# Performance work log

Measured on AMD Instinct MI355X. Metric: run time of the kernel, lower is better.

The kernel has to match this reference:

```python
import jax, jax.numpy as jnp
import numpy as np

N = 8192
F_IN = 128
F_OUT = 128
BLOCK = 64  # row block for the masked neighbor max-pool (keeps peak mem ~256MB)


def setup_inputs() -> dict:
    key = jax.random.key(0)
    k_in, k_adj, k_w, k_b = jax.random.split(key, 4)
    x = jax.random.normal(k_in, (N, F_IN), dtype=jnp.float32)
    adj = (jax.random.uniform(k_adj, (N, N)) < 0.01).astype(jnp.float32)
    adj = adj.at[jnp.arange(N), jnp.arange(N)].set(1.0)
    stdv = 1.0 / np.sqrt(F_OUT)
    weight = jax.random.uniform(k_w, (F_IN, F_OUT), minval=-stdv, maxval=stdv, dtype=jnp.float32)
    bias = jax.random.uniform(k_b, (F_OUT,), minval=-stdv, maxval=stdv, dtype=jnp.float32)
    return {"input": x, "adj": adj, "weight": weight, "bias": bias}


def _graph_pool(out, adj):
    # For each row i: max over features of out[j] where adj[i, j] != 0.
    # Blocked scan over rows to avoid materializing [N, N, F].
    neg = jnp.asarray(jnp.finfo(out.dtype).min, out.dtype)

    def body(_, adj_blk):  # adj_blk: [BLOCK, N]
        masked = jnp.where(adj_blk[:, :, None] != 0, out[None, :, :], neg)  # [BLOCK, N, F]
        return None, jnp.max(masked, axis=1)

    _, blocks = jax.lax.scan(body, None, adj.reshape(N // BLOCK, BLOCK, N))
    return blocks.reshape(N, out.shape[-1])


def reference(input, adj, weight, bias):
    h = input @ weight                       # [N, F_out]
    out = jnp.maximum(adj @ h + bias, 0.0)   # aggregate + bias + relu
    return _graph_pool(out, adj)             # per-node neighbor max-pool
```

## Files before the change

### kernel.cpp

```cpp
#include <hip/hip_runtime.h>
#include <float.h>

constexpr int N = 8192;
constexpr int F = 128;
constexpr int CAP = 256;

__global__ __launch_bounds__(128) void gemm_xw(const float* __restrict__ x,
                                               const float* __restrict__ w,
                                               float* __restrict__ h) {
    __shared__ float xs[8][F];
    const int f = threadIdx.x;
    const int row0 = blockIdx.x * 8;

    #pragma unroll
    for (int r = 0; r < 8; ++r) xs[r][f] = x[(size_t)(row0 + r) * F + f];
    __syncthreads();

    float acc[8];
    #pragma unroll
    for (int r = 0; r < 8; ++r) acc[r] = 0.f;

    for (int k = 0; k < F; ++k) {
        const float wk = w[(size_t)k * F + f];
        #pragma unroll
        for (int r = 0; r < 8; ++r) acc[r] += xs[r][k] * wk;
    }

    #pragma unroll
    for (int r = 0; r < 8; ++r) h[(size_t)(row0 + r) * F + f] = acc[r];
}

__global__ __launch_bounds__(256) void aggregate_relu_build_csr(
        const float* __restrict__ adj,
        const float* __restrict__ h,
        const float* __restrict__ bias,
        float* __restrict__ out2,
        unsigned short* __restrict__ csr_idx,
        int* __restrict__ csr_cnt) {
    __shared__ int idx[CAP];
    __shared__ int cnt;
    __shared__ float partial[F];

    const int tid  = threadIdx.x;
    const int lane = tid & 63;
    const int row  = blockIdx.x;

    if (tid == 0) cnt = 0;
    __syncthreads();

    const float4* arow = (const float4*)(adj + (size_t)row * N);
    float4 v[8];
    #pragma unroll
    for (int it = 0; it < 8; ++it) v[it] = arow[tid + it * 256];

    const unsigned long long lt = (1ull << lane) - 1ull;
    #pragma unroll
    for (int it = 0; it < 8; ++it) {
        const int j4 = 4 * (tid + it * 256);
        const float4 vv = v[it];
        const unsigned long long m0 = __ballot(vv.x != 0.f);
        const unsigned long long m1 = __ballot(vv.y != 0.f);
        const unsigned long long m2 = __ballot(vv.z != 0.f);
        const unsigned long long m3 = __ballot(vv.w != 0.f);
        const int c0 = __popcll(m0), c1 = __popcll(m1),
                  c2 = __popcll(m2), c3 = __popcll(m3);
        const int tot = c0 + c1 + c2 + c3;
        int base = 0;
        if (lane == 0 && tot) base = atomicAdd(&cnt, tot);
        base = __shfl(base, 0, 64);
        if (vv.x != 0.f) idx[base + __popcll(m0 & lt)] = j4 + 0;
        base += c0;
        if (vv.y != 0.f) idx[base + __popcll(m1 & lt)] = j4 + 1;
        base += c1;
        if (vv.z != 0.f) idx[base + __popcll(m2 & lt)] = j4 + 2;
        base += c2;
        if (vv.w != 0.f) idx[base + __popcll(m3 & lt)] = j4 + 3;
    }
    __syncthreads();

    const int n = min(cnt, CAP);

    if (tid == 0) csr_cnt[row] = n;
    if (tid < n) csr_idx[(size_t)row * CAP + tid] = (unsigned short)idx[tid];

    const int f = tid & (F - 1);
    const int half = tid >> 7;

    float acc = 0.f;
    int e = half;
    for (; e + 6 < n; e += 8) {
        const int j0 = idx[e], j1 = idx[e + 2], j2 = idx[e + 4], j3 = idx[e + 6];
        const float a0 = h[(size_t)j0 * F + f];
        const float a1 = h[(size_t)j1 * F + f];
        const float a2 = h[(size_t)j2 * F + f];
        const float a3 = h[(size_t)j3 * F + f];
        acc += (a0 + a1) + (a2 + a3);
    }
    for (; e < n; e += 2) acc += h[(size_t)idx[e] * F + f];

    if (half == 1) partial[f] = acc;
    __syncthreads();
    if (half == 0) {
        acc += partial[f];
        const float vb = acc + bias[f];
        out2[(size_t)row * F + f] = vb > 0.f ? vb : 0.f;
    }
}

__global__ __launch_bounds__(256) void neighbor_max_csr(
        const unsigned short* __restrict__ csr_idx,
        const int* __restrict__ csr_cnt,
        const float* __restrict__ out2,
        float* __restrict__ out) {
    __shared__ int idx[CAP];
    __shared__ float partial[F];

    const int tid = threadIdx.x;
    const int row = blockIdx.x;

    const int n = csr_cnt[row];
    if (tid < n) idx[tid] = csr_idx[(size_t)row * CAP + tid];
    __syncthreads();

    const int f = tid & (F - 1);
    const int half = tid >> 7;

    float acc = -FLT_MAX;
    int e = half;
    for (; e + 6 < n; e += 8) {
        const int j0 = idx[e], j1 = idx[e + 2], j2 = idx[e + 4], j3 = idx[e + 6];
        const float a0 = out2[(size_t)j0 * F + f];
        const float a1 = out2[(size_t)j1 * F + f];
        const float a2 = out2[(size_t)j2 * F + f];
        const float a3 = out2[(size_t)j3 * F + f];
        acc = fmaxf(acc, fmaxf(fmaxf(a0, a1), fmaxf(a2, a3)));
    }
    for (; e < n; e += 2) acc = fmaxf(acc, out2[(size_t)idx[e] * F + f]);

    if (half == 1) partial[f] = acc;
    __syncthreads();
    if (half == 0) {
        acc = fmaxf(acc, partial[f]);
        out[(size_t)row * F + f] = acc;
    }
}

extern "C" void kernel_launch(void* const* d_in, const int* in_sizes, int n_in,
                              void* d_out, int out_size, void* d_ws, size_t ws_size,
                              hipStream_t stream) {
    const float* x    = (const float*)d_in[0];
    const float* adj  = (const float*)d_in[1];
    const float* w    = (const float*)d_in[2];
    const float* bias = (const float*)d_in[3];
    float* out = (float*)d_out;

    float* h    = (float*)d_ws;
    float* out2 = h + (size_t)N * F;
    int* csr_cnt = (int*)(out2 + (size_t)N * F);
    unsigned short* csr_idx = (unsigned short*)(csr_cnt + N);

    gemm_xw<<<N / 8, 128, 0, stream>>>(x, w, h);
    aggregate_relu_build_csr<<<N, 256, 0, stream>>>(adj, h, bias, out2, csr_idx, csr_cnt);
    neighbor_max_csr<<<N, 256, 0, stream>>>(csr_idx, csr_cnt, out2, out);
}
```

Measured before the change: 401.7 us.

## Use bf16 MFMA for X@W and store intermediates in bf16

Replaces the scalar fp32 X@W kernel with a bf16 MFMA tile kernel, and stores h and the aggregated activations as bf16 so the gather kernels read half the bytes. The adjacency rows are now read with nontemporal loads so the streamed 256MB matrix does not pollute cache. The cost is reduced numerical precision in h and out2, which may matter for the tolerance check.

```diff
diff --git a/kernel.cpp b/kernel.cpp
--- a/kernel.cpp
+++ b/kernel.cpp
@@ -5,36 +5,84 @@
 constexpr int F = 128;
 constexpr int CAP = 256;
 
-__global__ __launch_bounds__(128) void gemm_xw(const float* __restrict__ x,
-                                               const float* __restrict__ w,
-                                               float* __restrict__ h) {
-    __shared__ float xs[8][F];
-    const int f = threadIdx.x;
-    const int row0 = blockIdx.x * 8;
-
-    #pragma unroll
-    for (int r = 0; r < 8; ++r) xs[r][f] = x[(size_t)(row0 + r) * F + f];
-    __syncthreads();
-
-    float acc[8];
-    #pragma unroll
-    for (int r = 0; r < 8; ++r) acc[r] = 0.f;
-
-    for (int k = 0; k < F; ++k) {
-        const float wk = w[(size_t)k * F + f];
-        #pragma unroll
-        for (int r = 0; r < 8; ++r) acc[r] += xs[r][k] * wk;
-    }
-
-    #pragma unroll
-    for (int r = 0; r < 8; ++r) h[(size_t)(row0 + r) * F + f] = acc[r];
+using short8 = __attribute__((ext_vector_type(8))) short;
+using float4v = __attribute__((ext_vector_type(4))) float;
+
+static __device__ inline unsigned short f2bf(float f) {
+    unsigned u = __float_as_uint(f);
+    u += 0x7fffu + ((u >> 16) & 1u);
+    return (unsigned short)(u >> 16);
+}
+static __device__ inline float bf2f(unsigned short s) {
+    return __uint_as_float((unsigned)s << 16);
+}
+
+constexpr int KP = 136;
+
+__global__ __launch_bounds__(256) void gemm_mfma(const float* __restrict__ x,
+                                                 const float* __restrict__ w,
+                                                 unsigned short* __restrict__ h) {
+    __shared__ unsigned short xs[64][KP];
+    __shared__ unsigned short wt[128][KP];
+
+    const int tid = threadIdx.x;
+    const int row0 = blockIdx.x * 64;
+
+    {
+        const float4* x4 = (const float4*)(x + (size_t)row0 * F);
+        #pragma unroll
+        for (int i = tid; i < 64 * F / 4; i += 256) {
+            const float4 v = x4[i];
+            const int r = (i * 4) >> 7, c = (i * 4) & 127;
+            xs[r][c + 0] = f2bf(v.x); xs[r][c + 1] = f2bf(v.y);
+            xs[r][c + 2] = f2bf(v.z); xs[r][c + 3] = f2bf(v.w);
+        }
+    }
+    {
+        const float4* w4 = (const float4*)w;
+        #pragma unroll
+        for (int i = tid; i < F * F / 4; i += 256) {
+            const float4 v = w4[i];
+            const int k = (i * 4) >> 7, n = (i * 4) & 127;
+            wt[n + 0][k] = f2bf(v.x); wt[n + 1][k] = f2bf(v.y);
+            wt[n + 2][k] = f2bf(v.z); wt[n + 3][k] = f2bf(v.w);
+        }
+    }
+    __syncthreads();
+
+    const int lane = tid & 63, wid = tid >> 6;
+    const int m = lane & 15, quad = lane >> 4;
+    const int m0 = wid * 16;
+
+    float4v acc[8];
+    #pragma unroll
+    for (int nt = 0; nt < 8; ++nt) acc[nt] = (float4v){0.f, 0.f, 0.f, 0.f};
+
+    #pragma unroll
+    for (int k0 = 0; k0 < F; k0 += 32) {
+        const short8 a = *(const short8*)&xs[m0 + m][k0 + quad * 8];
+        #pragma unroll
+        for (int nt = 0; nt < 8; ++nt) {
+            const short8 b = *(const short8*)&wt[nt * 16 + m][k0 + quad * 8];
+            acc[nt] = __builtin_amdgcn_mfma_f32_16x16x32_bf16(a, b, acc[nt], 0, 0, 0);
+        }
+    }
+
+    #pragma unroll
+    for (int nt = 0; nt < 8; ++nt)
+        #pragma unroll
+        for (int r = 0; r < 4; ++r) {
+            const int row = row0 + m0 + quad * 4 + r;
+            const int col = nt * 16 + m;
+            h[(size_t)row * F + col] = f2bf(acc[nt][r]);
+        }
 }
 
 __global__ __launch_bounds__(256) void aggregate_relu_build_csr(
         const float* __restrict__ adj,
-        const float* __restrict__ h,
+        const unsigned short* __restrict__ h,
         const float* __restrict__ bias,
-        float* __restrict__ out2,
+        unsigned short* __restrict__ out2,
         unsigned short* __restrict__ csr_idx,
         int* __restrict__ csr_cnt) {
     __shared__ int idx[CAP];
@@ -48,16 +96,16 @@
     if (tid == 0) cnt = 0;
     __syncthreads();
 
-    const float4* arow = (const float4*)(adj + (size_t)row * N);
-    float4 v[8];
-    #pragma unroll
-    for (int it = 0; it < 8; ++it) v[it] = arow[tid + it * 256];
+    const float4v* arow = (const float4v*)(adj + (size_t)row * N);
+    float4v v[8];
+    #pragma unroll
+    for (int it = 0; it < 8; ++it) v[it] = __builtin_nontemporal_load(arow + tid + it * 256);
 
     const unsigned long long lt = (1ull << lane) - 1ull;
     #pragma unroll
     for (int it = 0; it < 8; ++it) {
         const int j4 = 4 * (tid + it * 256);
-        const float4 vv = v[it];
+        const float4v vv = v[it];
         const unsigned long long m0 = __ballot(vv.x != 0.f);
         const unsigned long long m1 = __ballot(vv.y != 0.f);
         const unsigned long long m2 = __ballot(vv.z != 0.f);
@@ -90,27 +138,27 @@
     int e = half;
     for (; e + 6 < n; e += 8) {
         const int j0 = idx[e], j1 = idx[e + 2], j2 = idx[e + 4], j3 = idx[e + 6];
-        const float a0 = h[(size_t)j0 * F + f];
-        const float a1 = h[(size_t)j1 * F + f];
-        const float a2 = h[(size_t)j2 * F + f];
-        const float a3 = h[(size_t)j3 * F + f];
+        const float a0 = bf2f(h[(size_t)j0 * F + f]);
+        const float a1 = bf2f(h[(size_t)j1 * F + f]);
+        const float a2 = bf2f(h[(size_t)j2 * F + f]);
+        const float a3 = bf2f(h[(size_t)j3 * F + f]);
         acc += (a0 + a1) + (a2 + a3);
     }
-    for (; e < n; e += 2) acc += h[(size_t)idx[e] * F + f];
+    for (; e < n; e += 2) acc += bf2f(h[(size_t)idx[e] * F + f]);
 
     if (half == 1) partial[f] = acc;
     __syncthreads();
     if (half == 0) {
         acc += partial[f];
         const float vb = acc + bias[f];
-        out2[(size_t)row * F + f] = vb > 0.f ? vb : 0.f;
+        out2[(size_t)row * F + f] = f2bf(vb > 0.f ? vb : 0.f);
     }
 }
 
 __global__ __launch_bounds__(256) void neighbor_max_csr(
         const unsigned short* __restrict__ csr_idx,
         const int* __restrict__ csr_cnt,
-        const float* __restrict__ out2,
+        const unsigned short* __restrict__ out2,
         float* __restrict__ out) {
     __shared__ int idx[CAP];
     __shared__ float partial[F];
@@ -129,13 +177,13 @@
     int e = half;
     for (; e + 6 < n; e += 8) {
         const int j0 = idx[e], j1 = idx[e + 2], j2 = idx[e + 4], j3 = idx[e + 6];
-        const float a0 = out2[(size_t)j0 * F + f];
-        const float a1 = out2[(size_t)j1 * F + f];
-        const float a2 = out2[(size_t)j2 * F + f];
-        const float a3 = out2[(size_t)j3 * F + f];
+        const float a0 = bf2f(out2[(size_t)j0 * F + f]);
+        const float a1 = bf2f(out2[(size_t)j1 * F + f]);
+        const float a2 = bf2f(out2[(size_t)j2 * F + f]);
+        const float a3 = bf2f(out2[(size_t)j3 * F + f]);
         acc = fmaxf(acc, fmaxf(fmaxf(a0, a1), fmaxf(a2, a3)));
     }
-    for (; e < n; e += 2) acc = fmaxf(acc, out2[(size_t)idx[e] * F + f]);
+    for (; e < n; e += 2) acc = fmaxf(acc, bf2f(out2[(size_t)idx[e] * F + f]));
 
     if (half == 1) partial[f] = acc;
     __syncthreads();
@@ -154,12 +202,12 @@
     const float* bias = (const float*)d_in[3];
     float* out = (float*)d_out;
 
-    float* h    = (float*)d_ws;
-    float* out2 = h + (size_t)N * F;
+    unsigned short* h    = (unsigned short*)d_ws;
+    unsigned short* out2 = h + (size_t)N * F;
     int* csr_cnt = (int*)(out2 + (size_t)N * F);
     unsigned short* csr_idx = (unsigned short*)(csr_cnt + N);
 
-    gemm_xw<<<N / 8, 128, 0, stream>>>(x, w, h);
+    gemm_mfma<<<N / 64, 256, 0, stream>>>(x, w, h);
     aggregate_relu_build_csr<<<N, 256, 0, stream>>>(adj, h, bias, out2, csr_idx, csr_cnt);
     neighbor_max_csr<<<N, 256, 0, stream>>>(csr_idx, csr_cnt, out2, out);
 }
```

After: 386.5 us. 3.8% less time.
